# Kernel tuning notes

Hardware: AMD Instinct MI355X
Metric: run time of the kernel (lower is better)

## Reference

```python
import jax, jax.numpy as jnp
import numpy as np

FG_THRESH = 0.5  # box_fg_iou_thresh
BG_THRESH = 0.5  # box_bg_iou_thresh
BELOW_LOW = -1
BETWEEN = -2
WEIGHTS = np.array([0.1, 0.1, 0.2, 0.2], dtype=np.float32)


def _box_iou(g, p):
    # g: [M,4], p: [N,4] in (x1,y1,x2,y2) -> [M,N]
    area_g = (g[:, 2] - g[:, 0]) * (g[:, 3] - g[:, 1])
    area_p = (p[:, 2] - p[:, 0]) * (p[:, 3] - p[:, 1])
    lt = jnp.maximum(g[:, None, :2], p[None, :, :2])  # [M,N,2]
    rb = jnp.minimum(g[:, None, 2:], p[None, :, 2:])
    wh = jnp.clip(rb - lt, 0.0)
    inter = wh[..., 0] * wh[..., 1]
    return inter / (area_g[:, None] + area_p[None, :] - inter)


def setup_inputs() -> dict:
    key = jax.random.key(0)
    k1, k2, k3, k4, k5 = jax.random.split(key, 5)
    B, N, M = 4, 100000, 64
    # valid boxes: corner + positive extent (image ~1000x1000)
    p_xy = jax.random.uniform(k1, (B, N, 2), jnp.float32, 0.0, 800.0)
    p_wh = jax.random.uniform(k2, (B, N, 2), jnp.float32, 8.0, 200.0)
    proposals = jnp.concatenate([p_xy, p_xy + p_wh], axis=-1)
    g_xy = jax.random.uniform(k3, (B, M, 2), jnp.float32, 0.0, 800.0)
    g_wh = jax.random.uniform(k4, (B, M, 2), jnp.float32, 16.0, 200.0)
    gt_boxes = jnp.concatenate([g_xy, g_xy + g_wh], axis=-1)
    deltas = 0.1 * jax.random.normal(k5, (B, N, 4), jnp.float32)
    return {"proposals": proposals, "gt_boxes": gt_boxes, "deltas": deltas}


def reference(proposals, gt_boxes, deltas):
    w = jnp.asarray(WEIGHTS, dtype=proposals.dtype)

    def per_image(p, g):
        # Matcher: argmax over gt axis + threshold masking
        iou = _box_iou(g, p)                       # [M,N]
        matched_vals = iou.max(axis=0)             # [N]
        matches = iou.argmax(axis=0).astype(jnp.int32)
        matches = jnp.where(matched_vals < BG_THRESH, BELOW_LOW, matches)
        matches = jnp.where((matched_vals >= BG_THRESH) & (matched_vals < FG_THRESH), BETWEEN, matches)
        # BoxCoder.encoder against matched gt (clamped index gather)
        mg = g[jnp.clip(matches, 0)]               # [N,4]
        awh = p[:, 2:] - p[:, :2]
        axy = p[:, :2] + 0.5 * awh
        gwh = jnp.clip(mg[:, 2:] - mg[:, :2], 1.0)
        gxy = mg[:, :2] + 0.5 * gwh
        targets = jnp.concatenate([(gxy - axy) / awh, jnp.log(gwh / awh)], axis=-1) / w
        return matches, targets

    matches, targets = jax.vmap(per_image)(proposals, gt_boxes)

    awh = proposals[..., 2:] - proposals[..., :2]
    axy = proposals[..., :2] + 0.5 * awh
    sr = deltas * w
    ctr = axy + sr[..., :2] * awh
    wh = jnp.exp(sr[..., 2:]) * awh
    decoded = jnp.concatenate([ctr - 0.5 * wh, ctr + 0.5 * wh], axis=-1)  # [B,N,4]
    return decoded, targets, matches
```

## Files before the change

### kernel.cpp

```cpp
#include <hip/hip_runtime.h>

#define B_IMGS 4
#define N_PROP 100000
#define M_GT   64


__global__ __launch_bounds__(256) void roihead_kernel(
    const float* __restrict__ proposals,
    const float* __restrict__ gt,
    const float* __restrict__ deltas,
    float* __restrict__ out)
{
    __shared__ float4 g_s[M_GT];
    __shared__ float  ga_s[M_GT];

    const int b   = blockIdx.y;
    const int tid = threadIdx.x;

    if (tid < M_GT) {
        float4 g = reinterpret_cast<const float4*>(gt)[b * M_GT + tid];
        g_s[tid]  = g;
        ga_s[tid] = (g.z - g.x) * (g.w - g.y);
    }
    __syncthreads();

    const int n = blockIdx.x * blockDim.x + tid;
    if (n >= N_PROP) return;

    const long pi = (long)b * N_PROP + n;
    const float4 p = reinterpret_cast<const float4*>(proposals)[pi];

    float best_v = -1.0f;
    int   best_i = 0;
    {
#pragma clang fp contract(off)
        const float area_p = (p.z - p.x) * (p.w - p.y);
        for (int m = 0; m < M_GT; ++m) {
            const float4 g = g_s[m];
            const float ltx = fmaxf(g.x, p.x);
            const float lty = fmaxf(g.y, p.y);
            const float rbx = fminf(g.z, p.z);
            const float rby = fminf(g.w, p.w);
            const float wx  = fmaxf(rbx - ltx, 0.0f);
            const float wy  = fmaxf(rby - lty, 0.0f);
            const float inter = wx * wy;
            const float iou = inter / ((ga_s[m] + area_p) - inter);
            if (iou > best_v) { best_v = iou; best_i = m; }
        }
    }

    int match = best_i;
    if (best_v < 0.5f) match = -1;
    else if (best_v < 0.5f) match = -2;

    const float4 mg = g_s[match > 0 ? match : 0];
    const float aw = p.z - p.x;
    const float ah = p.w - p.y;
    const float ax = p.x + 0.5f * aw;
    const float ay = p.y + 0.5f * ah;
    const float gw = fmaxf(mg.z - mg.x, 1.0f);
    const float gh = fmaxf(mg.w - mg.y, 1.0f);
    const float gx = mg.x + 0.5f * gw;
    const float gy = mg.y + 0.5f * gh;

    float4 tgt;
    tgt.x = ((gx - ax) / aw) / 0.1f;
    tgt.y = ((gy - ay) / ah) / 0.1f;
    tgt.z = logf(gw / aw) / 0.2f;
    tgt.w = logf(gh / ah) / 0.2f;

    const float4 d = reinterpret_cast<const float4*>(deltas)[pi];
    const float sx = d.x * 0.1f;
    const float sy = d.y * 0.1f;
    const float sw = d.z * 0.2f;
    const float sh = d.w * 0.2f;
    const float cx = ax + sx * aw;
    const float cy = ay + sy * ah;
    const float w2 = expf(sw) * aw;
    const float h2 = expf(sh) * ah;

    float4 dec;
    dec.x = cx - 0.5f * w2;
    dec.y = cy - 0.5f * h2;
    dec.z = cx + 0.5f * w2;
    dec.w = cy + 0.5f * h2;

    float4* out4 = reinterpret_cast<float4*>(out);
    out4[pi] = dec;
    out4[(long)B_IMGS * N_PROP + pi] = tgt;
    out[(long)2 * B_IMGS * N_PROP * 4 + pi] = (float)match;
}

extern "C" void kernel_launch(void* const* d_in, const int* in_sizes, int n_in,
                              void* d_out, int out_size, void* d_ws, size_t ws_size,
                              hipStream_t stream) {
    const float* proposals = (const float*)d_in[0];
    const float* gt        = (const float*)d_in[1];
    const float* deltas    = (const float*)d_in[2];
    float* out = (float*)d_out;

    dim3 block(256);
    dim3 grid((N_PROP + 255) / 256, B_IMGS);
    roihead_kernel<<<grid, block, 0, stream>>>(proposals, gt, deltas, out);
}
```

Measured before the change: 90.32 us.

## Use fast reciprocal IoU argmax with exact fallback for near ties

Replaces the per-pair IEEE division in the IoU argmax loop with a hardware reciprocal approximation. It tracks the top two scores and reruns an exact-division pass only when they are nearly tied, then recomputes the exact IoU of the winner for thresholding. Ground-truth boxes are read directly from global memory as wave-uniform loads instead of staged in LDS, and the loop is unrolled. The cost is a rare second pass and a small risk of argmax mismatches for ties outside the tolerance.

```diff
diff --git a/kernel.cpp b/kernel.cpp
--- a/kernel.cpp
+++ b/kernel.cpp
@@ -11,15 +11,14 @@
     const float* __restrict__ deltas,
     float* __restrict__ out)
 {
-    __shared__ float4 g_s[M_GT];
-    __shared__ float  ga_s[M_GT];
+    __shared__ float ga_s[M_GT];
 
     const int b   = blockIdx.y;
     const int tid = threadIdx.x;
+    const float4* __restrict__ gt4 = reinterpret_cast<const float4*>(gt) + b * M_GT;
 
     if (tid < M_GT) {
-        float4 g = reinterpret_cast<const float4*>(gt)[b * M_GT + tid];
-        g_s[tid]  = g;
+        const float4 g = gt4[tid];
         ga_s[tid] = (g.z - g.x) * (g.w - g.y);
     }
     __syncthreads();
@@ -30,30 +29,51 @@
     const long pi = (long)b * N_PROP + n;
     const float4 p = reinterpret_cast<const float4*>(proposals)[pi];
 
-    float best_v = -1.0f;
-    int   best_i = 0;
+    float bv1 = -1.0f, bv2 = -1.0f; int bi = 0;
+    float ap;
     {
 #pragma clang fp contract(off)
-        const float area_p = (p.z - p.x) * (p.w - p.y);
+        ap = (p.z - p.x) * (p.w - p.y);
+#pragma unroll 8
         for (int m = 0; m < M_GT; ++m) {
-            const float4 g = g_s[m];
-            const float ltx = fmaxf(g.x, p.x);
-            const float lty = fmaxf(g.y, p.y);
-            const float rbx = fminf(g.z, p.z);
-            const float rby = fminf(g.w, p.w);
-            const float wx  = fmaxf(rbx - ltx, 0.0f);
-            const float wy  = fmaxf(rby - lty, 0.0f);
+            const float4 g  = gt4[m];
+            const float  ga = ga_s[m];
+            const float wx = fmaxf(fminf(g.z, p.z) - fmaxf(g.x, p.x), 0.0f);
+            const float wy = fmaxf(fminf(g.w, p.w) - fmaxf(g.y, p.y), 0.0f);
             const float inter = wx * wy;
-            const float iou = inter / ((ga_s[m] + area_p) - inter);
-            if (iou > best_v) { best_v = iou; best_i = m; }
+            const float uni   = (ga + ap) - inter;
+            const float a = inter * __builtin_amdgcn_rcpf(uni);
+            if (a > bv1)      { bv2 = bv1; bv1 = a; bi = m; }
+            else if (a > bv2) { bv2 = a; }
         }
     }
 
-    int match = best_i;
-    if (best_v < 0.5f) match = -1;
-    else if (best_v < 0.5f) match = -2;
+    float exact_v;
+    {
+#pragma clang fp contract(off)
+        const bool ambig = (bv2 > 0.0f) && ((bv1 - bv2) <= 2e-6f * bv1);
+        if (ambig) {
+            float bv = -1.0f; int nbi = 0;
+            for (int m = 0; m < M_GT; ++m) {
+                const float4 g = gt4[m];
+                const float wx = fmaxf(fminf(g.z, p.z) - fmaxf(g.x, p.x), 0.0f);
+                const float wy = fmaxf(fminf(g.w, p.w) - fmaxf(g.y, p.y), 0.0f);
+                const float inter = wx * wy;
+                const float iou = inter / ((ga_s[m] + ap) - inter);
+                if (iou > bv) { bv = iou; nbi = m; }
+            }
+            bi = nbi;
+        }
+        const float4 g = gt4[bi];
+        const float wx = fmaxf(fminf(g.z, p.z) - fmaxf(g.x, p.x), 0.0f);
+        const float wy = fmaxf(fminf(g.w, p.w) - fmaxf(g.y, p.y), 0.0f);
+        const float inter = wx * wy;
+        exact_v = inter / ((ga_s[bi] + ap) - inter);
+    }
 
-    const float4 mg = g_s[match > 0 ? match : 0];
+    const int match = (exact_v < 0.5f) ? -1 : bi;
+
+    const float4 mg = gt4[match < 0 ? 0 : match];
     const float aw = p.z - p.x;
     const float ah = p.w - p.y;
     const float ax = p.x + 0.5f * aw;
@@ -86,9 +106,10 @@
     dec.w = cy + 0.5f * h2;
 
     float4* out4 = reinterpret_cast<float4*>(out);
+    const long BN = (long)B_IMGS * N_PROP;
     out4[pi] = dec;
-    out4[(long)B_IMGS * N_PROP + pi] = tgt;
-    out[(long)2 * B_IMGS * N_PROP * 4 + pi] = (float)match;
+    out4[BN + pi] = tgt;
+    out[2 * BN * 4 + pi] = (float)match;
 }
 
 extern "C" void kernel_launch(void* const* d_in, const int* in_sizes, int n_in,
```

New measurement: 86.35 us. -4.4%, faster.
